# Optimization experiments

Hardware: AMD Instinct MI355X
Metric: run time of the kernel (lower is better)

The kernel has to match this reference:

```python
import math
import jax, jax.numpy as jnp
import numpy as np

B, S, D, H, DK, DV, L, DFF, V, NC, HID = 16, 512, 512, 8, 64, 64, 6, 2048, 32000, 5, 64


def setup_inputs() -> dict:
    key = jax.random.key(0)
    ks = jax.random.split(key, 32)
    def n(k, shape, scale=0.02):
        return jax.random.normal(k, shape, jnp.float32) * scale
    input_ids = jax.random.randint(ks[0], (B, S), 0, V).astype(jnp.int32)
    attention_mask = jnp.ones((B, S), jnp.bool_)
    emb = n(ks[1], (V, D)).at[0].set(0.0)  # padding_idx=0 row zeroed
    cls_token = jnp.zeros((D,), jnp.float32)
    return {
        "input_ids": input_ids,
        "attention_mask": attention_mask,
        "emb": emb,
        "cls_token": cls_token,
        "ln1_g": jnp.ones((L, D), jnp.float32), "ln1_b": jnp.zeros((L, D), jnp.float32),
        "ln2_g": jnp.ones((L, D), jnp.float32), "ln2_b": jnp.zeros((L, D), jnp.float32),
        "Wq": n(ks[2], (L, H, D, DK)), "bq": n(ks[3], (L, H, DK)),
        "Wk": n(ks[4], (L, H, D, DK)), "bk": n(ks[5], (L, H, DK)),
        "Wv": n(ks[6], (L, H, D, DV)), "bv": n(ks[7], (L, H, DV)),
        "Wo": n(ks[8], (L, H * DV, D)), "bo": n(ks[9], (L, D)),
        "W1": n(ks[10], (L, D, DFF)), "b1": n(ks[11], (L, DFF)),
        "W2": n(ks[12], (L, DFF, D)), "b2": n(ks[13], (L, D)),
        "Wc1": n(ks[14], (D, HID)), "bc1": n(ks[15], (HID,)),
        "Wc2": n(ks[16], (HID, NC)), "bc2": n(ks[17], (NC,)),
    }


def _layernorm(x, g, b, eps=1e-5):
    mu = jnp.mean(x, axis=-1, keepdims=True)
    var = jnp.var(x, axis=-1, keepdims=True)
    return (x - mu) * jax.lax.rsqrt(var + eps) * g + b


def _sinusoidal_pe(seq_len, d_model):
    pos = jnp.arange(seq_len, dtype=jnp.float32)[:, None]
    div = jnp.exp(jnp.arange(0, d_model, 2, dtype=jnp.float32) * (-math.log(10000.0) / d_model))
    pe = jnp.zeros((seq_len, d_model), jnp.float32)
    pe = pe.at[:, 0::2].set(jnp.sin(pos * div))
    pe = pe.at[:, 1::2].set(jnp.cos(pos * div))
    return pe


def _forward(input_ids, attention_mask, emb, cls_token,
             ln1_g, ln1_b, ln2_g, ln2_b,
             Wq, bq, Wk, bk, Wv, bv, Wo, bo,
             W1, b1, W2, b2, Wc1, bc1, Wc2, bc2):
    b, s = input_ids.shape
    x = emb[input_ids]                                     # [B,S,D]
    cls = jnp.broadcast_to(cls_token[None, None, :], (b, 1, x.shape[-1]))
    x = jnp.concatenate([cls, x], axis=1)                  # [B,S+1,D]
    full_mask = jnp.concatenate([jnp.ones((b, 1), jnp.bool_), attention_mask], axis=1)
    # pairwise attention mask [B, T, T]
    pair_mask = full_mask[:, None, :] & full_mask[:, :, None]
    x = x + _sinusoidal_pe(s + 1, x.shape[-1])[None]

    scale = 1.0 / math.sqrt(DK)

    def block(x, p):
        g1, be1, g2, be2, wq, bq_, wk, bk_, wv, bv_, wo, bo_, w1, bb1, w2, bb2 = p
        h = _layernorm(x, g1, be1)
        q = jnp.einsum('btd,hdk->bhtk', h, wq) + bq_[None, :, None, :]
        k = jnp.einsum('btd,hdk->bhtk', h, wk) + bk_[None, :, None, :]
        v = jnp.einsum('btd,hdv->bhtv', h, wv) + bv_[None, :, None, :]
        scores = jnp.einsum('bhqk,bhtk->bhqt', q, k) * scale
        scores = jnp.where(pair_mask[:, None, :, :], scores, -jnp.inf)
        attn = jax.nn.softmax(scores, axis=-1)
        o = jnp.einsum('bhqt,bhtv->bhqv', attn, v)          # [B,H,T,DV]
        o = o.transpose(0, 2, 1, 3).reshape(x.shape[0], x.shape[1], H * DV)
        x = x + o @ wo + bo_
        h2 = _layernorm(x, g2, be2)
        x = x + jnp.maximum(h2 @ w1 + bb1, 0.0) @ w2 + bb2
        return x, None

    params = (ln1_g, ln1_b, ln2_g, ln2_b, Wq, bq, Wk, bk, Wv, bv, Wo, bo, W1, b1, W2, b2)
    x, _ = jax.lax.scan(block, x, params)
    cls_out = x[:, 0]
    logits = jnp.maximum(cls_out @ Wc1 + bc1, 0.0) @ Wc2 + bc2
    return logits


def reference(input_ids, attention_mask, emb, cls_token,
              ln1_g, ln1_b, ln2_g, ln2_b,
              Wq, bq, Wk, bk, Wv, bv, Wo, bo,
              W1, b1, W2, b2, Wc1, bc1, Wc2, bc2):
    return _forward(input_ids, attention_mask, emb, cls_token,
                    ln1_g, ln1_b, ln2_g, ln2_b,
                    Wq, bq, Wk, bk, Wv, bv, Wo, bo,
                    W1, b1, W2, b2, Wc1, bc1, Wc2, bc2)
```

## Files before the change

### kernel.cpp

```cpp
#include <hip/hip_runtime.h>
#include <math.h>

#define DEV __device__ __forceinline__

typedef __attribute__((ext_vector_type(8))) short short8;
typedef __attribute__((ext_vector_type(4))) float f32x4;

DEV unsigned short f2bf(float f) {
  union { float f; unsigned int i; } v; v.f = f;
  unsigned int r = v.i + 0x7fffu + ((v.i >> 16) & 1u);
  return (unsigned short)(r >> 16);
}

DEV void lds16(const void* g, void* l) {
  __builtin_amdgcn_global_load_lds((__attribute__((address_space(1))) void*)(g),
                                   (__attribute__((address_space(3))) void*)(l), 16, 0, 0);
}


__global__ void transpose_g(const float* __restrict__ src, unsigned short* __restrict__ dst,
                            int Ksz, int Nsz) {
  __shared__ float tile[32][33];
  const int tx = threadIdx.x, ty = threadIdx.y;
  const int n0 = blockIdx.x * 32, k0 = blockIdx.y * 32;
  const size_t base = (size_t)blockIdx.z * Ksz * Nsz;
#pragma unroll
  for (int i = 0; i < 4; ++i)
    tile[ty + i * 8][tx] = src[base + (size_t)(k0 + ty + i * 8) * Nsz + n0 + tx];
  __syncthreads();
#pragma unroll
  for (int i = 0; i < 4; ++i)
    dst[base + (size_t)(n0 + ty + i * 8) * Ksz + k0 + tx] = f2bf(tile[tx][ty + i * 8]);
}

__global__ void pack_qkvT(const float* __restrict__ Wq, const float* __restrict__ Wk,
                          const float* __restrict__ Wv, unsigned short* __restrict__ dst) {
  __shared__ float tile[32][33];
  const int tx = threadIdx.x, ty = threadIdx.y;
  const int n0 = blockIdx.x * 32, k0 = blockIdx.y * 32, l = blockIdx.z;
  const int mat = n0 >> 9, hh = (n0 >> 6) & 7, dk0 = n0 & 63;
  const float* W = (mat == 0) ? Wq : (mat == 1) ? Wk : Wv;
  const float* Wl = W + ((size_t)l * 8 + hh) * 512 * 64;
#pragma unroll
  for (int i = 0; i < 4; ++i)
    tile[ty + i * 8][tx] = Wl[(size_t)(k0 + ty + i * 8) * 64 + dk0 + tx];
  __syncthreads();
#pragma unroll
  for (int i = 0; i < 4; ++i)
    dst[(size_t)l * 1536 * 512 + (size_t)(n0 + ty + i * 8) * 512 + k0 + tx] =
        f2bf(tile[tx][ty + i * 8]);
}

__global__ void pack_bias(const float* __restrict__ bq, const float* __restrict__ bk,
                          const float* __restrict__ bv, float* __restrict__ dst) {
  int i = blockIdx.x * 256 + threadIdx.x;
  if (i >= 6 * 1536) return;
  int l = i / 1536, c = i % 1536;
  float v = (c < 512) ? bq[l * 512 + c] : (c < 1024) ? bk[l * 512 + (c - 512)]
                                                     : bv[l * 512 + (c - 1024)];
  dst[i] = v;
}

__global__ void embed_kernel(const int* __restrict__ ids, const float* __restrict__ emb,
                             const float* __restrict__ cls, float* __restrict__ x) {
  int idx = blockIdx.x * 256 + threadIdx.x;
  int m = idx >> 9, d = idx & 511;
  int b = m / 513, t = m % 513;
  float v = (t == 0) ? cls[d] : emb[(size_t)ids[b * 512 + (t - 1)] * 512 + d];
  float fr = -(float)(d & ~1) * (9.2103403719761836f / 512.0f);
  float ang = (float)t * expf(fr);
  float pe = (d & 1) ? cosf(ang) : sinf(ang);
  x[idx] = v + pe;
}

__global__ __launch_bounds__(256) void ln_kernel(const float* __restrict__ x,
                                                 const float* __restrict__ g,
                                                 const float* __restrict__ bb,
                                                 unsigned short* __restrict__ h) {
  int wid = threadIdx.x >> 6, lane = threadIdx.x & 63;
  int m = blockIdx.x * 4 + wid;
  const float* xr = x + (size_t)m * 512;
  float4 a = *(const float4*)(xr + lane * 8);
  float4 c = *(const float4*)(xr + lane * 8 + 4);
  float s = a.x + a.y + a.z + a.w + c.x + c.y + c.z + c.w;
  float q = a.x * a.x + a.y * a.y + a.z * a.z + a.w * a.w +
            c.x * c.x + c.y * c.y + c.z * c.z + c.w * c.w;
#pragma unroll
  for (int d = 1; d < 64; d <<= 1) { s += __shfl_xor(s, d); q += __shfl_xor(q, d); }
  float mu = s * (1.f / 512.f);
  float var = q * (1.f / 512.f) - mu * mu;
  float rs = 1.f / sqrtf(var + 1e-5f);
  float4 g0 = *(const float4*)(g + lane * 8), g1 = *(const float4*)(g + lane * 8 + 4);
  float4 b0 = *(const float4*)(bb + lane * 8), b1 = *(const float4*)(bb + lane * 8 + 4);
  short8 ov;
  ov[0] = (short)f2bf((a.x - mu) * rs * g0.x + b0.x);
  ov[1] = (short)f2bf((a.y - mu) * rs * g0.y + b0.y);
  ov[2] = (short)f2bf((a.z - mu) * rs * g0.z + b0.z);
  ov[3] = (short)f2bf((a.w - mu) * rs * g0.w + b0.w);
  ov[4] = (short)f2bf((c.x - mu) * rs * g1.x + b1.x);
  ov[5] = (short)f2bf((c.y - mu) * rs * g1.y + b1.y);
  ov[6] = (short)f2bf((c.z - mu) * rs * g1.z + b1.z);
  ov[7] = (short)f2bf((c.w - mu) * rs * g1.w + b1.w);
  *(short8*)(h + (size_t)m * 512 + lane * 8) = ov;
}

template <int EPI>
__global__ __launch_bounds__(256) void gemm_bt(const unsigned short* __restrict__ A,
                                               const unsigned short* __restrict__ Bt,
                                               const float* __restrict__ bias,
                                               unsigned short* __restrict__ Cbf,
                                               float* __restrict__ Cres,
                                               unsigned short* __restrict__ vT,
                                               float* __restrict__ part,
                                               int M, int N, int K, int lda) {
  __shared__ __align__(16) unsigned short As[128 * 64];
  __shared__ __align__(16) unsigned short Bs[128 * 64];
  const int tid = threadIdx.x, w = tid >> 6, lane = tid & 63;
  const int l15 = lane & 15, l4 = lane >> 4;
  const int gx = gridDim.x;
  const int nwg = gx * gridDim.y;
  const int id = blockIdx.y * gx + blockIdx.x;
  const int xcd = id & 7, orig = id >> 3;
  const int qq = nwg >> 3, rr = nwg & 7;
  const int newid = (xcd < rr ? xcd * (qq + 1) : rr * (qq + 1) + (xcd - rr) * qq) + orig;
  const int m0 = (newid % gx) * 128, n0 = (newid / gx) * 128;
  const int wm = (w >> 1) * 64, wn = (w & 1) * 64;
  const int kbase = blockIdx.z * K;
  f32x4 acc[4][4] = {};
  const int nk = K >> 6;
  for (int kt = 0; kt < nk; ++kt) {
#pragma unroll
    for (int r = 0; r < 4; ++r) {
      int ol = (r * 4 + w) * 1024 + lane * 16;
      int ra = ol >> 7, cp = (ol >> 4) & 7;
      int co = ((cp ^ (ra & 7)) * 8) + kt * 64;
      lds16(A + (size_t)(m0 + ra) * lda + kbase + co, (char*)As + (r * 4 + w) * 1024);
      lds16(Bt + (size_t)(n0 + ra) * lda + kbase + co, (char*)Bs + (r * 4 + w) * 1024);
    }
    __syncthreads();
#pragma unroll
    for (int kk = 0; kk < 2; ++kk) {
      short8 af[4], bfr[4];
#pragma unroll
      for (int i = 0; i < 4; ++i) {
        int ar = wm + i * 16 + l15;
        af[i] = *(const short8*)&As[ar * 64 + (((kk * 4 + l4) ^ (ar & 7)) * 8)];
        int br = wn + i * 16 + l15;
        bfr[i] = *(const short8*)&Bs[br * 64 + (((kk * 4 + l4) ^ (br & 7)) * 8)];
      }
#pragma unroll
      for (int i = 0; i < 4; ++i)
#pragma unroll
        for (int j = 0; j < 4; ++j)
          acc[i][j] = __builtin_amdgcn_mfma_f32_16x16x32_bf16(af[i], bfr[j], acc[i][j], 0, 0, 0);
    }
    __syncthreads();
  }
  const bool z0 = (blockIdx.z == 0);
  const size_t MN = (size_t)M * N;
#pragma unroll
  for (int i = 0; i < 4; ++i) {
#pragma unroll
    for (int j = 0; j < 4; ++j) {
      const int gn = n0 + wn + j * 16 + l15;
      float bv = bias[gn];
      if constexpr (EPI == 2) {
        if (!z0) bv = 0.f;
      }
#pragma unroll
      for (int r = 0; r < 4; ++r) {
        const int gm = m0 + wm + i * 16 + l4 * 4 + r;
        if (gm < M) {
          float v = acc[i][j][r] + bv;
          if constexpr (EPI == 1) v = fmaxf(v, 0.f);
          if constexpr (EPI == 2) {
            if (z0) {
              Cres[(size_t)gm * N + gn] += v;
            } else {
              part[(size_t)(blockIdx.z - 1) * MN + (size_t)gm * N + gn] = v;
            }
          } else if constexpr (EPI == 3) {
            if (gn < 1024) {
              Cbf[(size_t)gm * N + gn] = f2bf(v);
            } else {
              int b = gm / 513, t = gm - b * 513;
              vT[(size_t)(b * 512 + (gn - 1024)) * 528 + t] = f2bf(v);
            }
          } else {
            Cbf[(size_t)gm * N + gn] = f2bf(v);
          }
        }
      }
    }
  }
}

__global__ __launch_bounds__(256) void reduce3(const float* __restrict__ p,
                                               float* __restrict__ x) {
  const size_t PN = 8208ull * 512;
  size_t i = ((size_t)blockIdx.x * 256 + threadIdx.x) * 4;
  float4 a = *(const float4*)(x + i);
  float4 b0 = *(const float4*)(p + i);
  float4 b1 = *(const float4*)(p + PN + i);
  float4 b2 = *(const float4*)(p + 2 * PN + i);
  a.x += b0.x + b1.x + b2.x;
  a.y += b0.y + b1.y + b2.y;
  a.z += b0.z + b1.z + b2.z;
  a.w += b0.w + b1.w + b2.w;
  *(float4*)(x + i) = a;
}

__global__ __launch_bounds__(256) void attn_kernel(const unsigned short* __restrict__ qkv,
                                                   const unsigned short* __restrict__ vT,
                                                   unsigned short* __restrict__ o) {
  const int qt = blockIdx.x, bh = blockIdx.y;
  const int b = bh >> 3, hh = bh & 7;
  const int tid = threadIdx.x, w = tid >> 6, lane = tid & 63;
  const int l15 = lane & 15, l4 = lane >> 4;
  __shared__ __align__(16) unsigned short Ks[64 * 64];
  __shared__ __align__(16) unsigned short Vs[64 * 64];
  __shared__ __align__(16) unsigned short Ps[64 * 72];
  const int q0 = qt * 64;
  const size_t qbase = (size_t)b * 513 * 1536;
  short8 qf[2];
  {
    const unsigned short* qp =
        qkv + qbase + (size_t)(q0 + w * 16 + l15) * 1536 + hh * 64 + l4 * 8;
    qf[0] = *(const short8*)qp;
    qf[1] = *(const short8*)(qp + 32);
  }
  f32x4 oacc[4] = {};
  float lpart[4] = {};
  for (int kvt = 0; kvt < 9; ++kvt) {
    const int kv0 = kvt * 64;
#pragma unroll
    for (int r = 0; r < 2; ++r) {
      int ol = (r * 4 + w) * 1024 + lane * 16;
      int rk = ol >> 7, cp = (ol >> 4) & 7;
      int sw = (cp ^ (rk & 7)) * 8;
      lds16(qkv + qbase + (size_t)(kv0 + rk) * 1536 + 512 + hh * 64 + sw,
            (char*)Ks + ol);
      lds16(vT + (size_t)(bh * 64 + rk) * 528 + kv0 + sw, (char*)Vs + ol);
    }
    __syncthreads();
    f32x4 sacc[4] = {};
#pragma unroll
    for (int kk = 0; kk < 2; ++kk)
#pragma unroll
      for (int nf = 0; nf < 4; ++nf) {
        int kr = nf * 16 + l15;
        short8 kf = *(const short8*)&Ks[kr * 64 + (((kk * 4 + l4) ^ (kr & 7)) * 8)];
        sacc[nf] = __builtin_amdgcn_mfma_f32_16x16x32_bf16(qf[kk], kf, sacc[nf], 0, 0, 0);
      }
#pragma unroll
    for (int nf = 0; nf < 4; ++nf) {
      const bool valid = (kv0 + nf * 16 + l15) < 513;
#pragma unroll
      for (int r = 0; r < 4; ++r) {
        float p = valid ? __expf(sacc[nf][r] * 0.125f) : 0.f;
        lpart[r] += p;
        Ps[(w * 16 + l4 * 4 + r) * 72 + nf * 16 + l15] = f2bf(p);
      }
    }
#pragma unroll
    for (int kk = 0; kk < 2; ++kk) {
      short8 pa = *(const short8*)&Ps[(w * 16 + l15) * 72 + kk * 32 + l4 * 8];
#pragma unroll
      for (int nf = 0; nf < 4; ++nf) {
        int dvr = nf * 16 + l15;
        short8 vf = *(const short8*)&Vs[dvr * 64 + (((kk * 4 + l4) ^ (dvr & 7)) * 8)];
        oacc[nf] = __builtin_amdgcn_mfma_f32_16x16x32_bf16(pa, vf, oacc[nf], 0, 0, 0);
      }
    }
    __syncthreads();
  }
#pragma unroll
  for (int d = 1; d < 16; d <<= 1)
#pragma unroll
    for (int r = 0; r < 4; ++r) lpart[r] += __shfl_xor(lpart[r], d);
#pragma unroll
  for (int nf = 0; nf < 4; ++nf)
#pragma unroll
    for (int r = 0; r < 4; ++r) {
      int q = q0 + w * 16 + l4 * 4 + r;
      if (q < 513) {
        float val = oacc[nf][r] / lpart[r];
        o[((size_t)b * 513 + q) * 512 + hh * 64 + nf * 16 + l15] = f2bf(val);
      }
    }
}

__global__ void cls_kernel(const float* __restrict__ x, const float* __restrict__ Wc1,
                           const float* __restrict__ bc1, const float* __restrict__ Wc2,
                           const float* __restrict__ bc2, float* __restrict__ out) {
  int b = blockIdx.x, j = threadIdx.x;
  const float* xr = x + (size_t)b * 513 * 512;
  float acc = bc1[j];
  for (int d = 0; d < 512; ++d) acc += xr[d] * Wc1[d * 64 + j];
  acc = fmaxf(acc, 0.f);
  __shared__ float hid[64];
  hid[j] = acc;
  __syncthreads();
  if (j < 5) {
    float lg = bc2[j];
#pragma unroll
    for (int d2 = 0; d2 < 64; ++d2) lg += hid[d2] * Wc2[d2 * 5 + j];
    out[b * 5 + j] = lg;
  }
}

extern "C" void kernel_launch(void* const* d_in, const int* in_sizes, int n_in,
                              void* d_out, int out_size, void* d_ws, size_t ws_size,
                              hipStream_t stream) {
  const int* ids = (const int*)d_in[0];
  const float* emb = (const float*)d_in[2];
  const float* cls = (const float*)d_in[3];
  const float* ln1g = (const float*)d_in[4];
  const float* ln1b = (const float*)d_in[5];
  const float* ln2g = (const float*)d_in[6];
  const float* ln2b = (const float*)d_in[7];
  const float* Wq = (const float*)d_in[8];
  const float* bq = (const float*)d_in[9];
  const float* Wk = (const float*)d_in[10];
  const float* bk = (const float*)d_in[11];
  const float* Wv = (const float*)d_in[12];
  const float* bv = (const float*)d_in[13];
  const float* Wo = (const float*)d_in[14];
  const float* bo = (const float*)d_in[15];
  const float* W1 = (const float*)d_in[16];
  const float* b1 = (const float*)d_in[17];
  const float* W2 = (const float*)d_in[18];
  const float* b2 = (const float*)d_in[19];
  const float* Wc1 = (const float*)d_in[20];
  const float* bc1 = (const float*)d_in[21];
  const float* Wc2 = (const float*)d_in[22];
  const float* bc2 = (const float*)d_in[23];

  char* ws = (char*)d_ws;
  size_t off = 0;
  auto alloc = [&](size_t bytes) {
    char* p = ws + off;
    off += (bytes + 255) & ~(size_t)255;
    return p;
  };
  const size_t QKV_ELEMS = 8320ull * 1536;
  const size_t VT_ELEMS = 16ull * 512 * 528 + 528;
  const size_t FFN_ELEMS = 8320ull * 2048;
  const size_t BIGU = (QKV_ELEMS + VT_ELEMS > FFN_ELEMS) ? QKV_ELEMS + VT_ELEMS : FFN_ELEMS;

  unsigned short* wqkvT = (unsigned short*)alloc(6ull * 1536 * 512 * 2);
  unsigned short* woT = (unsigned short*)alloc(6ull * 512 * 512 * 2);
  unsigned short* w1T = (unsigned short*)alloc(6ull * 2048 * 512 * 2);
  unsigned short* w2T = (unsigned short*)alloc(6ull * 512 * 2048 * 2);
  float* bqkv = (float*)alloc(6ull * 1536 * 4);
  float* x = (float*)alloc(8208ull * 512 * 4);
  unsigned short* hbuf = (unsigned short*)alloc(8320ull * 512 * 2);
  unsigned short* obuf = (unsigned short*)alloc(8320ull * 512 * 2);
  unsigned short* big = (unsigned short*)alloc(BIGU * 2);
  float* fpart = (float*)alloc(3ull * 8208 * 512 * 4);
  unsigned short* vT = big + QKV_ELEMS;
  if (off > ws_size) return;

  hipMemsetAsync(hbuf + 8208ull * 512, 0, 112ull * 512 * 2, stream);
  hipMemsetAsync(obuf + 8208ull * 512, 0, 112ull * 512 * 2, stream);
  hipMemsetAsync(big + 8208ull * 1536, 0, 112ull * 1536 * 2, stream);
  hipMemsetAsync(vT, 0, VT_ELEMS * 2, stream);

  pack_qkvT<<<dim3(48, 16, 6), dim3(32, 8), 0, stream>>>(Wq, Wk, Wv, wqkvT);
  transpose_g<<<dim3(16, 16, 6), dim3(32, 8), 0, stream>>>(Wo, woT, 512, 512);
  transpose_g<<<dim3(64, 16, 6), dim3(32, 8), 0, stream>>>(W1, w1T, 512, 2048);
  transpose_g<<<dim3(16, 64, 6), dim3(32, 8), 0, stream>>>(W2, w2T, 2048, 512);
  pack_bias<<<36, 256, 0, stream>>>(bq, bk, bv, bqkv);
  embed_kernel<<<16416, 256, 0, stream>>>(ids, emb, cls, x);

  for (int l = 0; l < 6; ++l) {
    ln_kernel<<<2052, 256, 0, stream>>>(x, ln1g + l * 512, ln1b + l * 512, hbuf);
    gemm_bt<3><<<dim3(65, 12), 256, 0, stream>>>(hbuf, wqkvT + (size_t)l * 1536 * 512,
                                                 bqkv + l * 1536, big, nullptr, vT,
                                                 nullptr, 8208, 1536, 512, 512);
    attn_kernel<<<dim3(9, 128), 256, 0, stream>>>(big, vT, obuf);
    gemm_bt<2><<<dim3(65, 4), 256, 0, stream>>>(obuf, woT + (size_t)l * 512 * 512,
                                                bo + l * 512, nullptr, x, nullptr,
                                                nullptr, 8208, 512, 512, 512);
    ln_kernel<<<2052, 256, 0, stream>>>(x, ln2g + l * 512, ln2b + l * 512, hbuf);
    gemm_bt<1><<<dim3(65, 16), 256, 0, stream>>>(hbuf, w1T + (size_t)l * 2048 * 512,
                                                 b1 + l * 2048, big, nullptr, nullptr,
                                                 nullptr, 8208, 2048, 512, 512);
    gemm_bt<2><<<dim3(65, 4, 4), 256, 0, stream>>>(big, w2T + (size_t)l * 512 * 2048,
                                                   b2 + l * 512, nullptr, x, nullptr,
                                                   fpart, 8208, 512, 512, 2048);
    reduce3<<<4104, 256, 0, stream>>>(fpart, x);
  }
  cls_kernel<<<16, 64, 0, stream>>>(x, Wc1, bc1, Wc2, bc2, (float*)d_out);
}
```

Before: 1.377 ms.

## Fuse split-K reduction into next LayerNorm and add 128x256 wide GEMM tiles

The separate reduce3 pass after the W2 split-K GEMM is removed. The next layer's LN1 kernel now sums the three partial buffers into x, writes x back, and normalises it in one pass; a single reduce3 remains after the last layer. A new 512-thread GEMM with 128x256 tiles replaces the 128x128 kernel for the QKV, W1 and W2 projections. This halves the N-grid and raises B-tile reuse per block, at the cost of more LDS per block and fewer blocks, which may lower occupancy.

```diff
diff --git a/kernel.cpp b/kernel.cpp
--- a/kernel.cpp
+++ b/kernel.cpp
@@ -73,15 +73,30 @@
   x[idx] = v + pe;
 }
 
-__global__ __launch_bounds__(256) void ln_kernel(const float* __restrict__ x,
+template <int FUSE>
+__global__ __launch_bounds__(256) void ln_kernel(float* __restrict__ x,
                                                  const float* __restrict__ g,
                                                  const float* __restrict__ bb,
-                                                 unsigned short* __restrict__ h) {
+                                                 unsigned short* __restrict__ h,
+                                                 const float* __restrict__ part) {
   int wid = threadIdx.x >> 6, lane = threadIdx.x & 63;
   int m = blockIdx.x * 4 + wid;
-  const float* xr = x + (size_t)m * 512;
+  float* xr = x + (size_t)m * 512;
   float4 a = *(const float4*)(xr + lane * 8);
   float4 c = *(const float4*)(xr + lane * 8 + 4);
+  if constexpr (FUSE) {
+    const size_t PN = 8208ull * 512;
+    const float* p = part + (size_t)m * 512 + lane * 8;
+    float4 q0 = *(const float4*)(p),          q0b = *(const float4*)(p + 4);
+    float4 q1 = *(const float4*)(p + PN),     q1b = *(const float4*)(p + PN + 4);
+    float4 q2 = *(const float4*)(p + 2 * PN), q2b = *(const float4*)(p + 2 * PN + 4);
+    a.x += q0.x + q1.x + q2.x;  a.y += q0.y + q1.y + q2.y;
+    a.z += q0.z + q1.z + q2.z;  a.w += q0.w + q1.w + q2.w;
+    c.x += q0b.x + q1b.x + q2b.x;  c.y += q0b.y + q1b.y + q2b.y;
+    c.z += q0b.z + q1b.z + q2b.z;  c.w += q0b.w + q1b.w + q2b.w;
+    *(float4*)(xr + lane * 8) = a;
+    *(float4*)(xr + lane * 8 + 4) = c;
+  }
   float s = a.x + a.y + a.z + a.w + c.x + c.y + c.z + c.w;
   float q = a.x * a.x + a.y * a.y + a.z * a.z + a.w * a.w +
             c.x * c.x + c.y * c.y + c.z * c.z + c.w * c.w;
@@ -102,6 +117,51 @@
   ov[6] = (short)f2bf((c.z - mu) * rs * g1.z + b1.z);
   ov[7] = (short)f2bf((c.w - mu) * rs * g1.w + b1.w);
   *(short8*)(h + (size_t)m * 512 + lane * 8) = ov;
+}
+
+template <int EPI>
+DEV void gemm_epilogue(f32x4 (&acc)[4][4], const float* __restrict__ bias,
+                       unsigned short* __restrict__ Cbf, float* __restrict__ Cres,
+                       unsigned short* __restrict__ vT, float* __restrict__ part,
+                       int M, int N, int m0, int n0, int wm, int wn, int l15, int l4,
+                       int bz) {
+  const bool z0 = (bz == 0);
+  const size_t MN = (size_t)M * N;
+#pragma unroll
+  for (int i = 0; i < 4; ++i) {
+#pragma unroll
+    for (int j = 0; j < 4; ++j) {
+      const int gn = n0 + wn + j * 16 + l15;
+      float bv = bias[gn];
+      if constexpr (EPI == 2) {
+        if (!z0) bv = 0.f;
+      }
+#pragma unroll
+      for (int r = 0; r < 4; ++r) {
+        const int gm = m0 + wm + i * 16 + l4 * 4 + r;
+        if (gm < M) {
+          float v = acc[i][j][r] + bv;
+          if constexpr (EPI == 1) v = fmaxf(v, 0.f);
+          if constexpr (EPI == 2) {
+            if (z0) {
+              Cres[(size_t)gm * N + gn] += v;
+            } else {
+              part[(size_t)(bz - 1) * MN + (size_t)gm * N + gn] = v;
+            }
+          } else if constexpr (EPI == 3) {
+            if (gn < 1024) {
+              Cbf[(size_t)gm * N + gn] = f2bf(v);
+            } else {
+              int b = gm / 513, t = gm - b * 513;
+              vT[(size_t)(b * 512 + (gn - 1024)) * 528 + t] = f2bf(v);
+            }
+          } else {
+            Cbf[(size_t)gm * N + gn] = f2bf(v);
+          }
+        }
+      }
+    }
+  }
 }
 
 template <int EPI>
@@ -156,43 +216,72 @@
     }
     __syncthreads();
   }
-  const bool z0 = (blockIdx.z == 0);
-  const size_t MN = (size_t)M * N;
-#pragma unroll
-  for (int i = 0; i < 4; ++i) {
-#pragma unroll
-    for (int j = 0; j < 4; ++j) {
-      const int gn = n0 + wn + j * 16 + l15;
-      float bv = bias[gn];
-      if constexpr (EPI == 2) {
-        if (!z0) bv = 0.f;
-      }
-#pragma unroll
-      for (int r = 0; r < 4; ++r) {
-        const int gm = m0 + wm + i * 16 + l4 * 4 + r;
-        if (gm < M) {
-          float v = acc[i][j][r] + bv;
-          if constexpr (EPI == 1) v = fmaxf(v, 0.f);
-          if constexpr (EPI == 2) {
-            if (z0) {
-              Cres[(size_t)gm * N + gn] += v;
-            } else {
-              part[(size_t)(blockIdx.z - 1) * MN + (size_t)gm * N + gn] = v;
-            }
-          } else if constexpr (EPI == 3) {
-            if (gn < 1024) {
-              Cbf[(size_t)gm * N + gn] = f2bf(v);
-            } else {
-              int b = gm / 513, t = gm - b * 513;
-              vT[(size_t)(b * 512 + (gn - 1024)) * 528 + t] = f2bf(v);
-            }
-          } else {
-            Cbf[(size_t)gm * N + gn] = f2bf(v);
-          }
-        }
-      }
-    }
-  }
+  gemm_epilogue<EPI>(acc, bias, Cbf, Cres, vT, part, M, N, m0, n0, wm, wn, l15, l4,
+                     blockIdx.z);
+}
+
+template <int EPI>
+__global__ __launch_bounds__(512) void gemm_wide(const unsigned short* __restrict__ A,
+                                                 const unsigned short* __restrict__ Bt,
+                                                 const float* __restrict__ bias,
+                                                 unsigned short* __restrict__ Cbf,
+                                                 float* __restrict__ Cres,
+                                                 unsigned short* __restrict__ vT,
+                                                 float* __restrict__ part,
+                                                 int M, int N, int K, int lda) {
+  __shared__ __align__(16) unsigned short As[128 * 64];
+  __shared__ __align__(16) unsigned short Bs[256 * 64];
+  const int tid = threadIdx.x, w = tid >> 6, lane = tid & 63;
+  const int l15 = lane & 15, l4 = lane >> 4;
+  const int gx = gridDim.x;
+  const int nwg = gx * gridDim.y;
+  const int id = blockIdx.y * gx + blockIdx.x;
+  const int xcd = id & 7, orig = id >> 3;
+  const int qq = nwg >> 3, rr = nwg & 7;
+  const int newid = (xcd < rr ? xcd * (qq + 1) : rr * (qq + 1) + (xcd - rr) * qq) + orig;
+  const int m0 = (newid % gx) * 128, n0 = (newid / gx) * 256;
+  const int wm = (w >> 2) * 64, wn = (w & 3) * 64;
+  const int kbase = blockIdx.z * K;
+  f32x4 acc[4][4] = {};
+  const int nk = K >> 6;
+  for (int kt = 0; kt < nk; ++kt) {
+#pragma unroll
+    for (int r = 0; r < 2; ++r) {
+      int s = r * 8 + w;
+      int ol = s * 1024 + lane * 16;
+      int ra = ol >> 7, cp = (ol >> 4) & 7;
+      int co = ((cp ^ (ra & 7)) * 8) + kt * 64;
+      lds16(A + (size_t)(m0 + ra) * lda + kbase + co, (char*)As + s * 1024);
+    }
+#pragma unroll
+    for (int r = 0; r < 4; ++r) {
+      int s = r * 8 + w;
+      int ol = s * 1024 + lane * 16;
+      int rb = ol >> 7, cp = (ol >> 4) & 7;
+      int co = ((cp ^ (rb & 7)) * 8) + kt * 64;
+      lds16(Bt + (size_t)(n0 + rb) * lda + kbase + co, (char*)Bs + s * 1024);
+    }
+    __syncthreads();
+#pragma unroll
+    for (int kk = 0; kk < 2; ++kk) {
+      short8 af[4], bfr[4];
+#pragma unroll
+      for (int i = 0; i < 4; ++i) {
+        int ar = wm + i * 16 + l15;
+        af[i] = *(const short8*)&As[ar * 64 + (((kk * 4 + l4) ^ (ar & 7)) * 8)];
+        int br = wn + i * 16 + l15;
+        bfr[i] = *(const short8*)&Bs[br * 64 + (((kk * 4 + l4) ^ (br & 7)) * 8)];
+      }
+#pragma unroll
+      for (int i = 0; i < 4; ++i)
+#pragma unroll
+        for (int j = 0; j < 4; ++j)
+          acc[i][j] = __builtin_amdgcn_mfma_f32_16x16x32_bf16(af[i], bfr[j], acc[i][j], 0, 0, 0);
+    }
+    __syncthreads();
+  }
+  gemm_epilogue<EPI>(acc, bias, Cbf, Cres, vT, part, M, N, m0, n0, wm, wn, l15, l4,
+                     blockIdx.z);
 }
 
 __global__ __launch_bounds__(256) void reduce3(const float* __restrict__ p,
@@ -374,22 +463,28 @@
   embed_kernel<<<16416, 256, 0, stream>>>(ids, emb, cls, x);
 
   for (int l = 0; l < 6; ++l) {
-    ln_kernel<<<2052, 256, 0, stream>>>(x, ln1g + l * 512, ln1b + l * 512, hbuf);
-    gemm_bt<3><<<dim3(65, 12), 256, 0, stream>>>(hbuf, wqkvT + (size_t)l * 1536 * 512,
-                                                 bqkv + l * 1536, big, nullptr, vT,
-                                                 nullptr, 8208, 1536, 512, 512);
+    if (l == 0)
+      ln_kernel<0><<<2052, 256, 0, stream>>>(x, ln1g + l * 512, ln1b + l * 512, hbuf,
+                                             nullptr);
+    else
+      ln_kernel<1><<<2052, 256, 0, stream>>>(x, ln1g + l * 512, ln1b + l * 512, hbuf,
+                                             fpart);
+    gemm_wide<3><<<dim3(65, 6), 512, 0, stream>>>(hbuf, wqkvT + (size_t)l * 1536 * 512,
+                                                  bqkv + l * 1536, big, nullptr, vT,
+                                                  nullptr, 8208, 1536, 512, 512);
     attn_kernel<<<dim3(9, 128), 256, 0, stream>>>(big, vT, obuf);
     gemm_bt<2><<<dim3(65, 4), 256, 0, stream>>>(obuf, woT + (size_t)l * 512 * 512,
                                                 bo + l * 512, nullptr, x, nullptr,
                                                 nullptr, 8208, 512, 512, 512);
-    ln_kernel<<<2052, 256, 0, stream>>>(x, ln2g + l * 512, ln2b + l * 512, hbuf);
-    gemm_bt<1><<<dim3(65, 16), 256, 0, stream>>>(hbuf, w1T + (size_t)l * 2048 * 512,
-                                                 b1 + l * 2048, big, nullptr, nullptr,
-                                                 nullptr, 8208, 2048, 512, 512);
-    gemm_bt<2><<<dim3(65, 4, 4), 256, 0, stream>>>(big, w2T + (size_t)l * 512 * 2048,
-                                                   b2 + l * 512, nullptr, x, nullptr,
-                                                   fpart, 8208, 512, 512, 2048);
-    reduce3<<<4104, 256, 0, stream>>>(fpart, x);
-  }
+    ln_kernel<0><<<2052, 256, 0, stream>>>(x, ln2g + l * 512, ln2b + l * 512, hbuf,
+                                           nullptr);
+    gemm_wide<1><<<dim3(65, 8), 512, 0, stream>>>(hbuf, w1T + (size_t)l * 2048 * 512,
+                                                  b1 + l * 2048, big, nullptr, nullptr,
+                                                  nullptr, 8208, 2048, 512, 512);
+    gemm_wide<2><<<dim3(65, 2, 4), 512, 0, stream>>>(big, w2T + (size_t)l * 512 * 2048,
+                                                     b2 + l * 512, nullptr, x, nullptr,
+                                                     fpart, 8208, 512, 512, 2048);
+  }
+  reduce3<<<4104, 256, 0, stream>>>(fpart, x);
   cls_kernel<<<16, 64, 0, stream>>>(x, Wc1, bc1, Wc2, bc2, (float*)d_out);
 }
```

New measurement: 1.292 ms. 1.07x faster.
